# Kernel optimization log

Measured on AMD Instinct MI355X. Metric: run time of the kernel, lower is better.

The kernel has to match this reference:

```python
import jax, jax.numpy as jnp
import numpy as np

H, D = 8, 32
IN, HID, OUT = 256, 256, 128
N_PAR, N_FIG, N_TAB, N_CIT = 100000, 20000, 20000, 50000
E = 200000


def setup_inputs() -> dict:
    key = jax.random.key(0)
    ks = iter(jax.random.split(key, 80))
    def nrm(shape, s=0.05):
        return jax.random.normal(next(ks), shape, dtype=jnp.float32) * s
    def ridx(n):
        return jax.random.randint(next(ks), (E,), 0, n, dtype=jnp.int32)
    inp = {
        'x_par': nrm((N_PAR, IN), 1.0), 'x_fig': nrm((N_FIG, IN), 1.0),
        'x_tab': nrm((N_TAB, IN), 1.0), 'x_cit': nrm((N_CIT, IN), 1.0),
    }
    for t in ['par', 'fig', 'tab', 'cit']:
        inp[f'Wp_{t}'] = nrm((IN, HID)); inp[f'bp_{t}'] = nrm((HID,))
    for et in ['pf', 'fp', 'pt', 'tp', 'pc', 'cp']:
        inp[f'a_{et}_s'] = nrm((H, D)); inp[f'a_{et}_d'] = nrm((H, D))
    inp['k_w'] = nrm((HID, HID)); inp['k_b'] = nrm((HID,)); inp['q'] = nrm((HID,))
    for t in ['par', 'fig', 'tab', 'cit']:
        inp[f'Wh_{t}'] = nrm((HID, OUT)); inp[f'bh_{t}'] = nrm((OUT,))
    inp['cls_w'] = nrm((2 * OUT, 1)); inp['cls_b'] = nrm((1,))
    inp['pf_src'] = ridx(N_PAR); inp['pf_dst'] = ridx(N_FIG)
    inp['fp_src'] = ridx(N_FIG); inp['fp_dst'] = ridx(N_PAR)
    inp['pt_src'] = ridx(N_PAR); inp['pt_dst'] = ridx(N_TAB)
    inp['tp_src'] = ridx(N_TAB); inp['tp_dst'] = ridx(N_PAR)
    inp['pc_src'] = ridx(N_PAR); inp['pc_dst'] = ridx(N_CIT)
    inp['cp_src'] = ridx(N_CIT); inp['cp_dst'] = ridx(N_PAR)
    inp['target_node_idx'] = 5
    return inp


def _agg(xs, xd, si, di, a_s, a_d, n_dst):
    # HANConv metapath aggregation: GAT-style attention + per-dst softmax + scatter-sum + relu
    as_ = jnp.einsum('nhd,hd->nh', xs, a_s)            # [Ns,H]
    ad_ = jnp.einsum('nhd,hd->nh', xd, a_d)            # [Nd,H]
    alpha = jax.nn.leaky_relu(as_[si] + ad_[di], 0.2)  # [E,H]
    m = jax.ops.segment_max(alpha, di, num_segments=n_dst)
    m = jnp.where(jnp.isfinite(m), m, 0.0)
    ex = jnp.exp(alpha - m[di])
    den = jax.ops.segment_sum(ex, di, num_segments=n_dst)
    w = ex / (den[di] + 1e-16)
    out = jax.ops.segment_sum(xs[si] * w[:, :, None], di, num_segments=n_dst)  # [Nd,H,D]
    return jax.nn.relu(out.reshape(n_dst, H * D))


def _group(outs, q, kw, kb):
    # HANConv semantic (metapath-level) attention
    st = jnp.stack(outs)                               # [M,N,F]
    kmean = jnp.tanh(st @ kw + kb).mean(axis=1)        # [M,F]
    attn = jax.nn.softmax(kmean @ q)                   # [M]
    return jnp.einsum('m,mnf->nf', attn, st)


def reference(x_par, x_fig, x_tab, x_cit,
              Wp_par, bp_par, Wp_fig, bp_fig, Wp_tab, bp_tab, Wp_cit, bp_cit,
              a_pf_s, a_pf_d, a_fp_s, a_fp_d, a_pt_s, a_pt_d,
              a_tp_s, a_tp_d, a_pc_s, a_pc_d, a_cp_s, a_cp_d,
              k_w, k_b, q,
              Wh_par, bh_par, Wh_fig, bh_fig, Wh_tab, bh_tab, Wh_cit, bh_cit,
              cls_w, cls_b,
              pf_src, pf_dst, fp_src, fp_dst, pt_src, pt_dst,
              tp_src, tp_dst, pc_src, pc_dst, cp_src, cp_dst,
              target_node_idx):
    # per-node-type input projection
    h_par = (x_par @ Wp_par + bp_par).reshape(-1, H, D)
    h_fig = (x_fig @ Wp_fig + bp_fig).reshape(-1, H, D)
    h_tab = (x_tab @ Wp_tab + bp_tab).reshape(-1, H, D)
    h_cit = (x_cit @ Wp_cit + bp_cit).reshape(-1, H, D)
    # per-metapath message passing, grouped per destination node type
    o_fig = _group([_agg(h_par, h_fig, pf_src, pf_dst, a_pf_s, a_pf_d, N_FIG)], q, k_w, k_b)
    o_tab = _group([_agg(h_par, h_tab, pt_src, pt_dst, a_pt_s, a_pt_d, N_TAB)], q, k_w, k_b)
    o_cit = _group([_agg(h_par, h_cit, pc_src, pc_dst, a_pc_s, a_pc_d, N_CIT)], q, k_w, k_b)
    o_par = _group([
        _agg(h_fig, h_par, fp_src, fp_dst, a_fp_s, a_fp_d, N_PAR),
        _agg(h_tab, h_par, tp_src, tp_dst, a_tp_s, a_tp_d, N_PAR),
        _agg(h_cit, h_par, cp_src, cp_dst, a_cp_s, a_cp_d, N_PAR),
    ], q, k_w, k_b)
    # output heads (table/cited_paper heads computed in the original but unused for scores)
    par_emb = o_par @ Wh_par + bh_par
    fig_emb = o_fig @ Wh_fig + bh_fig
    _ = o_tab @ Wh_tab + bh_tab
    _ = o_cit @ Wh_cit + bh_cit
    # pairwise classifier: target figure embedding broadcast against every paragraph
    target = fig_emb[target_node_idx]
    comb = jnp.concatenate(
        [jnp.broadcast_to(target[None, :], (par_emb.shape[0], OUT)), par_emb], axis=1)
    scores = (comb @ cls_w + cls_b)[:, 0]
    return scores
```

## Files before the change

kernel.cpp:

```cpp
#include <hip/hip_runtime.h>
#include <hip/hip_bf16.h>
#include <math.h>

typedef float f32x4 __attribute__((ext_vector_type(4)));
typedef short bf16x8 __attribute__((ext_vector_type(8)));

#define NPAR 100000
#define NFIG 20000
#define NTAB 20000
#define NCIT 50000
#define NEDGE 200000
#define CAP 32
#define PFCAP 79

__device__ __forceinline__ unsigned short f2b(float f) {
    union { float f; unsigned u; } x; x.f = f;
    unsigned r = x.u + 0x7FFFu + ((x.u >> 16) & 1u);
    return (unsigned short)(r >> 16);
}
__device__ __forceinline__ float b2f(unsigned short b) {
    union { unsigned u; float f; } x; x.u = ((unsigned)b) << 16; return x.f;
}
__device__ __forceinline__ float fast_tanh(float x) {
    float e = __expf(2.f * x);
    return 1.f - 2.f * __builtin_amdgcn_rcpf(e + 1.f);
}
__device__ __forceinline__ void async_copy16(const unsigned short* g, unsigned short* l) {
    __builtin_amdgcn_global_load_lds(
        (const __attribute__((address_space(1))) unsigned int*)g,
        (__attribute__((address_space(3))) unsigned int*)l, 16, 0, 0);
}

__global__ void k_transpose5(const float* __restrict__ W0, const float* __restrict__ W1,
                             const float* __restrict__ W2, const float* __restrict__ W3,
                             const float* __restrict__ W4, unsigned short* __restrict__ WT) {
    int b = blockIdx.x, which = b >> 8, k = b & 255, n = threadIdx.x;
    const float* W = which == 0 ? W0 : which == 1 ? W1 : which == 2 ? W2 : which == 3 ? W3 : W4;
    WT[(size_t)which * 65536 + n * 256 + k] = f2b(W[k * 256 + n]);
}

__global__ void k_precompute(const float* __restrict__ WhF, const float* __restrict__ bhF,
                             const float* __restrict__ WhP, const float* __restrict__ bhP,
                             const float* __restrict__ clsw, const float* __restrict__ clsb,
                             float* __restrict__ u, float* __restrict__ v, float* __restrict__ smallb) {
    int t = threadIdx.x;
    float su = 0.f, sv = 0.f;
    for (int j = 0; j < 128; ++j) {
        su += WhF[t * 128 + j] * clsw[j];
        sv += WhP[t * 128 + j] * clsw[128 + j];
    }
    u[t] = su; v[t] = sv;
    if (t == 0) {
        float c = clsb[0];
        for (int j = 0; j < 128; ++j) c += bhF[j] * clsw[j] + bhP[j] * clsw[128 + j];
        smallb[264] = c;
    }
}

__global__ void k_edges(const int* __restrict__ d0, const int* __restrict__ d1,
                        const int* __restrict__ d2, int* __restrict__ count,
                        int* __restrict__ elist,
                        const int* __restrict__ psrc, const int* __restrict__ pdst,
                        const int* __restrict__ tgtp, int* __restrict__ mlist) {
    int b = blockIdx.x;
    int m = b / 782;
    int e = (b - m * 782) * 256 + threadIdx.x;
    if (e >= NEDGE) return;
    if (m < 3) {
        const int* dst = m == 0 ? d0 : m == 1 ? d1 : d2;
        int d = dst[e];
        int* cnt = count + (size_t)m * NPAR;
        int* el = elist + (size_t)m * NPAR * CAP;
        int slot = atomicAdd(&cnt[d], 1);
        if (slot < CAP) el[(size_t)d * CAP + slot] = e;
    } else {
        if (pdst[e] == tgtp[0]) {
            int slot = atomicAdd(&mlist[0], 1);
            if (slot < PFCAP) mlist[1 + slot] = psrc[e];
        }
    }
}

struct ProjPack {
    const float* X[4];
    const unsigned short* WT[4];
    const float* bias[4];
    unsigned short* H[4];
    const float* av[16];
    float* ov[16];
    int nrows[4];
    int bbase[4];
    int nv[4];
};

#define LOADA(k0, A0, A1) do { \
    const float4* _p = reinterpret_cast<const float4*>(Arow + (k0)); \
    A0 = _p[0]; A1 = _p[1]; } while (0)
#define WRITEA(buf, A0, A1) do { \
    __align__(16) unsigned short _t[8]; \
    _t[0] = f2b(A0.x); _t[1] = f2b(A0.y); _t[2] = f2b(A0.z); _t[3] = f2b(A0.w); \
    _t[4] = f2b(A1.x); _t[5] = f2b(A1.y); _t[6] = f2b(A1.z); _t[7] = f2b(A1.w); \
    *reinterpret_cast<uint4*>(&As[buf][arow * 32 + acol]) = *reinterpret_cast<const uint4*>(_t); } while (0)

__global__ __launch_bounds__(512, 4) void k_gemm_proj(ProjPack p) {
    __shared__ __align__(16) unsigned short As[2][128 * 32];
    __shared__ __align__(16) unsigned short Bs[2][256 * 32];
    int bid = blockIdx.x;
    int ty = (bid >= p.bbase[1]) + (bid >= p.bbase[2]) + (bid >= p.bbase[3]);
    int m0 = (bid - p.bbase[ty]) * 128;
    const float* Xf = p.X[ty];
    const unsigned short* B = p.WT[ty];
    unsigned short* Hout = p.H[ty];
    int Nrows = p.nrows[ty];
    int nv = p.nv[ty];

    int t = threadIdx.x, l = t & 63, w = t >> 6;
    int wm = (w >> 2) * 64, wn = (w & 3) * 64;
    int lr = l & 15, hi = l >> 4;
    int arow = t >> 2, acol = (t & 3) * 8;
    int arow_c = m0 + arow; if (arow_c > Nrows - 1) arow_c = Nrows - 1;
    const float* Arow = Xf + (size_t)arow_c * 256 + acol;
    f32x4 acc[4][4] = {};
    float4 aP0, aP1, aQ0, aQ1;

    auto stageB = [&](int buf, int k0) {
#pragma unroll
        for (int i = 0; i < 2; ++i) {
            int rowb = w * 32 + i * 16;
            async_copy16(B + (size_t)(rowb + (l >> 2)) * 256 + k0 + (l & 3) * 8,
                         &Bs[buf][rowb * 32]);
        }
    };

    LOADA(0, aP0, aP1);
    stageB(0, 0);
    WRITEA(0, aP0, aP1);
    LOADA(32, aQ0, aQ1);
    asm volatile("s_waitcnt vmcnt(2) lgkmcnt(0)" ::: "memory");
    __builtin_amdgcn_s_barrier();

#pragma unroll
    for (int ks = 0; ks < 8; ++ks) {
        int cur = ks & 1;
        if (ks < 7) stageB(cur ^ 1, (ks + 1) * 32);
        if (ks < 6) {
            if ((ks & 1) == 0) LOADA((ks + 2) * 32, aP0, aP1);
            else               LOADA((ks + 2) * 32, aQ0, aQ1);
        }
        bf16x8 af[4], bfr[4];
#pragma unroll
        for (int mm = 0; mm < 4; ++mm)
            af[mm] = *reinterpret_cast<const bf16x8*>(&As[cur][(wm + mm * 16 + lr) * 32 + hi * 8]);
#pragma unroll
        for (int nn = 0; nn < 4; ++nn)
            bfr[nn] = *reinterpret_cast<const bf16x8*>(&Bs[cur][(wn + nn * 16 + lr) * 32 + hi * 8]);
#pragma unroll
        for (int mm = 0; mm < 4; ++mm)
#pragma unroll
            for (int nn = 0; nn < 4; ++nn)
                acc[mm][nn] = __builtin_amdgcn_mfma_f32_16x16x32_bf16(bfr[nn], af[mm], acc[mm][nn], 0, 0, 0);
        if (ks < 7) {
            if ((ks & 1) == 0) WRITEA(cur ^ 1, aQ0, aQ1);
            else               WRITEA(cur ^ 1, aP0, aP1);
            if (ks < 6) asm volatile("s_waitcnt vmcnt(2) lgkmcnt(0)" ::: "memory");
            else        asm volatile("s_waitcnt vmcnt(0) lgkmcnt(0)" ::: "memory");
            __builtin_amdgcn_s_barrier();
        }
    }

    __syncthreads();
    float* sattp = (float*)&As[0][0];
    unsigned short* Hst = &Bs[0][0];

    float4 bv4[4], av4[4][4];
#pragma unroll
    for (int nn = 0; nn < 4; ++nn)
        bv4[nn] = *reinterpret_cast<const float4*>(p.bias[ty] + wn + nn * 16 + hi * 4);
#pragma unroll
    for (int v = 0; v < 4; ++v)
        if (v < nv) {
            const float* A = p.av[ty * 4 + v];
#pragma unroll
            for (int nn = 0; nn < 4; ++nn)
                av4[v][nn] = *reinterpret_cast<const float4*>(A + wn + nn * 16 + hi * 4);
        }
    int h0 = (w & 3) * 2;
#pragma unroll
    for (int mm = 0; mm < 4; ++mm) {
        int lrow = wm + mm * 16 + lr;
        float sv[4][2] = {};
#pragma unroll
        for (int nn = 0; nn < 4; ++nn) {
            float c0 = acc[mm][nn][0] + bv4[nn].x;
            float c1 = acc[mm][nn][1] + bv4[nn].y;
            float c2 = acc[mm][nn][2] + bv4[nn].z;
            float c3 = acc[mm][nn][3] + bv4[nn].w;
#pragma unroll
            for (int v = 0; v < 4; ++v)
                if (v < nv)
                    sv[v][nn >> 1] += c0 * av4[v][nn].x + c1 * av4[v][nn].y +
                                      c2 * av4[v][nn].z + c3 * av4[v][nn].w;
        }
#pragma unroll
        for (int v = 0; v < 4; ++v)
            if (v < nv) {
#pragma unroll
                for (int hp = 0; hp < 2; ++hp) {
                    float s = sv[v][hp];
                    s += __shfl_xor(s, 16); s += __shfl_xor(s, 32);
                    if (hi == 0) sattp[v * 1024 + lrow * 8 + h0 + hp] = s;
                }
            }
    }

    if (ty != 0) {
        for (int hf = 0; hf < 2; ++hf) {
            if ((w >> 2) == hf) {
#pragma unroll
                for (int mm = 0; mm < 4; ++mm) {
                    int lr2 = mm * 16 + lr;
                    int swz = (lr2 & 7) << 4;
#pragma unroll
                    for (int nn = 0; nn < 4; ++nn) {
                        int colb = (wn + nn * 16 + hi * 4) * 2;
                        ushort4 o;
                        o.x = f2b(acc[mm][nn][0] + bv4[nn].x);
                        o.y = f2b(acc[mm][nn][1] + bv4[nn].y);
                        o.z = f2b(acc[mm][nn][2] + bv4[nn].z);
                        o.w = f2b(acc[mm][nn][3] + bv4[nn].w);
                        *reinterpret_cast<ushort4*>((char*)Hst + lr2 * 512 + (colb ^ swz)) = o;
                    }
                }
            }
            __syncthreads();
            {
                int row = t >> 3;
                int g = m0 + hf * 64 + row;
                if (g < Nrows) {
                    int swz = (row & 7) << 4;
#pragma unroll
                    for (int pass = 0; pass < 4; ++pass) {
                        int c = (t & 7) + pass * 8;
                        uint4 val = *reinterpret_cast<const uint4*>(
                            (const char*)Hst + row * 512 + ((c * 16) ^ swz));
                        *reinterpret_cast<uint4*>(Hout + (size_t)g * 256 + c * 8) = val;
                    }
                }
            }
            __syncthreads();
        }
    } else {
        __syncthreads();
    }

    for (int i = t; i < nv * 1024; i += 512) {
        int v = i >> 10, rem = i & 1023, lrow = rem >> 3, hd = rem & 7;
        int g = m0 + lrow;
        if (g < Nrows) p.ov[ty * 4 + v][(size_t)g * 8 + hd] = sattp[v * 1024 + lrow * 8 + hd];
    }
}

__global__ void k_pf_proj(const int* __restrict__ mlist, const float* __restrict__ Xp,
                          const unsigned short* __restrict__ WTp, const float* __restrict__ bp,
                          unsigned short* __restrict__ Hs) {
    int b = blockIdx.x;
    int cnt = mlist[0]; if (cnt > PFCAP) cnt = PFCAP;
    if (b >= cnt) return;
    int s = mlist[1 + b];
    __shared__ float xr[256];
    int t = threadIdx.x;
    xr[t] = Xp[(size_t)s * 256 + t];
    __syncthreads();
    const unsigned short* wrow = WTp + (size_t)t * 256;
    float acc = bp[t];
    for (int k = 0; k < 256; k += 8) {
        uint4 wv = *reinterpret_cast<const uint4*>(wrow + k);
        unsigned wsv[4] = { wv.x, wv.y, wv.z, wv.w };
#pragma unroll
        for (int j = 0; j < 4; ++j) {
            acc += xr[k + j * 2]     * b2f((unsigned short)(wsv[j] & 0xffffu));
            acc += xr[k + j * 2 + 1] * b2f((unsigned short)(wsv[j] >> 16));
        }
    }
    Hs[(size_t)b * 256 + t] = f2b(acc);
}

struct GKPack {
    const int* src[3]; const int* count[3]; const int* elist[3];
    const unsigned short* H[3]; const float* as_[3]; const float* ad_[3];
    const unsigned short* Bw; const float* kb; const float* v;
    float* ksum[3]; float* gout[3];
};
__global__ __launch_bounds__(512, 4) void k_gather_kmean(GKPack p) {
    __shared__ __align__(16) unsigned short Ar[32 * 256];
    __shared__ __align__(16) unsigned short Bs[2][256 * 32];
    int bid = blockIdx.x;
    int m = bid / 3125, b2 = bid - m * 3125;
    const int* src = p.src[m];
    const int* count = p.count[m];
    const int* elist = p.elist[m];
    const unsigned short* Hsrc = p.H[m];
    const float* as_ = p.as_[m];
    const float* ad_ = p.ad_[m];
    const unsigned short* Bw = p.Bw;
    int t = threadIdx.x, l = t & 63, w = t >> 6;
    int m0 = b2 * 32;
    int lg = l & 15, gb = l & 48;
    float* ks_rep = p.ksum[m] + (size_t)(b2 & 7) * 256;

    auto stageB = [&](int buf, int k0) {
#pragma unroll
        for (int i = 0; i < 2; ++i) {
            int rowb = w * 32 + i * 16;
            async_copy16(Bw + (size_t)(rowb + (l >> 2)) * 256 + k0 + (((l & 3) ^ ((l >> 2) & 3)) * 8),
                         &Bs[buf][rowb * 32]);
        }
    };
    stageB(0, 0);

    int ld = w * 4 + (l >> 4);
    int d = m0 + ld;
    int cnt = count[d]; if (cnt > CAP) cnt = CAP;
    int e1 = (lg < cnt) ? elist[(size_t)d * CAP + lg] : -1;
    int e2 = (lg + 16 < cnt) ? elist[(size_t)d * CAP + lg + 16] : -1;
    int s1 = (e1 >= 0) ? src[e1] : 0;
    int s2 = (e2 >= 0) ? src[e2] : 0;
    float adh = ad_[d * 8 + (lg >> 1)];

    float4 vv0 = *reinterpret_cast<const float4*>(p.v + lg * 16);
    float4 vv1 = *reinterpret_cast<const float4*>(p.v + lg * 16 + 4);
    float4 vv2 = *reinterpret_cast<const float4*>(p.v + lg * 16 + 8);
    float4 vv3 = *reinterpret_cast<const float4*>(p.v + lg * 16 + 12);
    float vr[16] = { vv0.x, vv0.y, vv0.z, vv0.w, vv1.x, vv1.y, vv1.z, vv1.w,
                     vv2.x, vv2.y, vv2.z, vv2.w, vv3.x, vv3.y, vv3.z, vv3.w };

    {
        float ar[16];
#pragma unroll
        for (int k = 0; k < 16; ++k) ar[k] = 0.f;
        float den = 0.f;
        int sC = __shfl(s1, gb);
        const uint4* hp0 = reinterpret_cast<const uint4*>(Hsrc + (size_t)sC * 256 + lg * 16);
        uint4 hA = {}, hB = {};
        float asv = 0.f;
        if (cnt > 0) { hA = hp0[0]; hB = hp0[1]; asv = as_[sC * 8 + (lg >> 1)]; }
        for (int i = 0; i < cnt; ++i) {
            int iN = i + 1;
            uint4 nA = {}, nB = {};
            float nas = 0.f;
            if (iN < cnt) {
                int sN = (iN < 16) ? __shfl(s1, gb + (iN & 15)) : __shfl(s2, gb + ((iN - 16) & 15));
                const uint4* np = reinterpret_cast<const uint4*>(Hsrc + (size_t)sN * 256 + lg * 16);
                nA = np[0]; nB = np[1];
                nas = as_[sN * 8 + (lg >> 1)];
            }
            float al = asv + adh;
            al = al > 0.f ? al : 0.2f * al;
            float ex = __expf(al); den += ex;
            unsigned wds[8] = { hA.x, hA.y, hA.z, hA.w, hB.x, hB.y, hB.z, hB.w };
#pragma unroll
            for (int k = 0; k < 8; ++k) {
                ar[k * 2]     += ex * b2f((unsigned short)(wds[k] & 0xffffu));
                ar[k * 2 + 1] += ex * b2f((unsigned short)(wds[k] >> 16));
            }
            hA = nA; hB = nB; asv = nas;
        }
        float inv = 1.f / (den + 1e-16f);
        float gs = 0.f;
        __align__(16) unsigned short ob[16];
#pragma unroll
        for (int k = 0; k < 16; ++k) {
            float r = fmaxf(ar[k] * inv, 0.f);
            gs += r * vr[k];
            ob[k] = f2b(r);
        }
        int u0 = (lg * 2) ^ (ld & 7), u1 = (lg * 2 + 1) ^ (ld & 7);
        *reinterpret_cast<uint4*>(&Ar[ld * 256 + u0 * 8]) = *reinterpret_cast<const uint4*>(ob);
        *reinterpret_cast<uint4*>(&Ar[ld * 256 + u1 * 8]) = *reinterpret_cast<const uint4*>(ob + 8);
        gs += __shfl_xor(gs, 1); gs += __shfl_xor(gs, 2); gs += __shfl_xor(gs, 4); gs += __shfl_xor(gs, 8);
        if (lg == 0) p.gout[m][d] = gs;
    }
    __syncthreads();

    int wm = (w >> 2) * 16, wn = (w & 3) * 64, lr = l & 15, hi = l >> 4;
    f32x4 acc[4] = {};
#pragma unroll
    for (int ks = 0; ks < 8; ++ks) {
        int cur = ks & 1;
        if (ks < 7) stageB(cur ^ 1, (ks + 1) * 32);
        bf16x8 af, bfr[4];
        {
            int rr = wm + lr;
            af = *reinterpret_cast<const bf16x8*>(&Ar[rr * 256 + (((ks * 4 + hi) ^ (rr & 7)) * 8)]);
        }
#pragma unroll
        for (int nn = 0; nn < 4; ++nn) {
            int row = wn + nn * 16 + lr;
            bfr[nn] = *reinterpret_cast<const bf16x8*>(&Bs[cur][row * 32 + ((hi ^ (row & 3)) * 8)]);
        }
#pragma unroll
        for (int nn = 0; nn < 4; ++nn)
            acc[nn] = __builtin_amdgcn_mfma_f32_16x16x32_bf16(af, bfr[nn], acc[nn], 0, 0, 0);
        if (ks < 7) {
            asm volatile("s_waitcnt vmcnt(0)" ::: "memory");
            __builtin_amdgcn_s_barrier();
        }
    }
#pragma unroll
    for (int nn = 0; nn < 4; ++nn) {
        int col = wn + nn * 16 + lr;
        float kbv = p.kb[col];
        float cs = 0.f;
#pragma unroll
        for (int r = 0; r < 4; ++r)
            cs += fast_tanh(acc[nn][r] + kbv);
        cs += __shfl_xor(cs, 16);
        cs += __shfl_xor(cs, 32);
        if (hi == 0) atomicAdd(&ks_rep[col], cs);
    }
}

__global__ void k_pf_acc(const int* __restrict__ mlist, const int* __restrict__ tgtp,
                         const unsigned short* __restrict__ Hs,
                         const float* __restrict__ as_pf, const float* __restrict__ ad_pf,
                         float* __restrict__ smallb) {
    __shared__ float sacc[4][256];
    __shared__ float sden[4][8];
    int t = threadIdx.x, w = t >> 6, l = t & 63;
    int tgt = tgtp[0];
    int cnt = mlist[0]; if (cnt > PFCAP) cnt = PFCAP;
    int h = l >> 3;
    float adh = ad_pf[tgt * 8 + h];
    float a0 = 0.f, a1 = 0.f, a2 = 0.f, a3 = 0.f, den = 0.f;
    for (int i = w; i < cnt; i += 4) {
        int s = mlist[1 + i];
        float al = as_pf[s * 8 + h] + adh;
        al = al > 0.f ? al : 0.2f * al;
        float ex = __expf(al);
        ushort4 hv = *reinterpret_cast<const ushort4*>(&Hs[(size_t)i * 256 + l * 4]);
        a0 += ex * b2f(hv.x); a1 += ex * b2f(hv.y); a2 += ex * b2f(hv.z); a3 += ex * b2f(hv.w);
        den += ex;
    }
    sacc[w][l * 4 + 0] = a0; sacc[w][l * 4 + 1] = a1;
    sacc[w][l * 4 + 2] = a2; sacc[w][l * 4 + 3] = a3;
    if ((l & 7) == 0) sden[w][h] = den;
    __syncthreads();
    smallb[t] = sacc[0][t] + sacc[1][t] + sacc[2][t] + sacc[3][t];
    if (t < 8) smallb[256 + t] = sden[0][t] + sden[1][t] + sden[2][t] + sden[3][t];
}

__global__ void k_finalize(const float* __restrict__ kacc, const float* __restrict__ q,
                           const float* __restrict__ u, float* __restrict__ smallb) {
    __shared__ float red[256];
    __shared__ float sm[3];
    int t = threadIdx.x;
    float qv = q[t];
    for (int m = 0; m < 3; ++m) {
        float acc = 0.f;
#pragma unroll
        for (int rep = 0; rep < 8; ++rep) acc += kacc[m * 2048 + rep * 256 + t];
        red[t] = acc * qv;
        __syncthreads();
        for (int s = 128; s > 0; s >>= 1) { if (t < s) red[t] += red[t + s]; __syncthreads(); }
        if (t == 0) sm[m] = red[0] / (float)NPAR;
        __syncthreads();
    }
    float den = smallb[256 + (t >> 5)];
    float rt = fmaxf(smallb[t] / (den + 1e-16f), 0.f);
    red[t] = rt * u[t];
    __syncthreads();
    for (int s = 128; s > 0; s >>= 1) { if (t < s) red[t] += red[t + s]; __syncthreads(); }
    if (t == 0) {
        float mx = fmaxf(sm[0], fmaxf(sm[1], sm[2]));
        float e0 = expf(sm[0] - mx), e1 = expf(sm[1] - mx), e2 = expf(sm[2] - mx);
        float sd = e0 + e1 + e2;
        smallb[265] = e0 / sd; smallb[266] = e1 / sd; smallb[267] = e2 / sd;
        smallb[268] = red[0] + smallb[264];
    }
}

__global__ void k_scores(const float* __restrict__ g, const float* __restrict__ smallb,
                         float* __restrict__ out) {
    int i = blockIdx.x * 256 + threadIdx.x;
    if (i >= NPAR) return;
    out[i] = smallb[268] + smallb[265] * g[i] + smallb[266] * g[NPAR + i] + smallb[267] * g[2 * NPAR + i];
}

extern "C" void kernel_launch(void* const* d_in, const int* in_sizes, int n_in,
                              void* d_out, int out_size, void* d_ws, size_t ws_size,
                              hipStream_t stream) {
    char* base = (char*)d_ws;
    size_t off = 0;
    auto alloc = [&](size_t b) -> void* { void* p = base + off; off += (b + 255) & ~(size_t)255; return p; };

    unsigned short* Hsmall = (unsigned short*)alloc((size_t)PFCAP * 256 * 2);
    unsigned short* h_fig = (unsigned short*)alloc((size_t)NFIG * 256 * 2);
    unsigned short* h_tab = (unsigned short*)alloc((size_t)NTAB * 256 * 2);
    unsigned short* h_cit = (unsigned short*)alloc((size_t)NCIT * 256 * 2);
    unsigned short* WTall = (unsigned short*)alloc((size_t)5 * 65536 * 2);
    unsigned short* WT_par = WTall, *WT_fig = WTall + 65536, *WT_tab = WTall + 2 * 65536,
                  *WT_cit = WTall + 3 * 65536, *kwT = WTall + 4 * 65536;
    float* as_pf = (float*)alloc((size_t)NPAR * 8 * 4);
    float* ad_fp = (float*)alloc((size_t)NPAR * 8 * 4);
    float* ad_tp = (float*)alloc((size_t)NPAR * 8 * 4);
    float* ad_cp = (float*)alloc((size_t)NPAR * 8 * 4);
    float* as_fp = (float*)alloc((size_t)NFIG * 8 * 4);
    float* ad_pf = (float*)alloc((size_t)NFIG * 8 * 4);
    float* as_tp = (float*)alloc((size_t)NTAB * 8 * 4);
    float* as_cp = (float*)alloc((size_t)NCIT * 8 * 4);
    float* gbuf  = (float*)alloc((size_t)3 * NPAR * 4);
    int* count3  = (int*)alloc((size_t)3 * NPAR * 4);
    int* elist3  = (int*)alloc((size_t)3 * NPAR * CAP * 4);
    float* kacc  = (float*)alloc((size_t)3 * 8 * 256 * 4);
    float* smallb = (float*)alloc(512 * 4);
    int* mlist   = (int*)alloc((1 + PFCAP) * 4);
    float* uvec  = (float*)alloc(256 * 4);
    float* vvec  = (float*)alloc(256 * 4);

    hipMemsetAsync(kacc, 0, 24576 + 2048 + 512, stream);
    hipMemsetAsync(count3, 0, (size_t)3 * NPAR * 4, stream);

    k_transpose5<<<5 * 256, 256, 0, stream>>>((const float*)d_in[4], (const float*)d_in[6],
                                              (const float*)d_in[8], (const float*)d_in[10],
                                              (const float*)d_in[24], WTall);

    k_precompute<<<1, 256, 0, stream>>>((const float*)d_in[29], (const float*)d_in[30],
                                        (const float*)d_in[27], (const float*)d_in[28],
                                        (const float*)d_in[35], (const float*)d_in[36],
                                        uvec, vvec, smallb);

    k_edges<<<4 * 782, 256, 0, stream>>>((const int*)d_in[40], (const int*)d_in[44],
                                         (const int*)d_in[48], count3, elist3,
                                         (const int*)d_in[37], (const int*)d_in[38],
                                         (const int*)d_in[49], mlist);
    k_pf_proj<<<PFCAP, 256, 0, stream>>>(mlist, (const float*)d_in[0], WT_par,
                                         (const float*)d_in[5], Hsmall);

    ProjPack pp;
    pp.X[0] = (const float*)d_in[0]; pp.X[1] = (const float*)d_in[1];
    pp.X[2] = (const float*)d_in[2]; pp.X[3] = (const float*)d_in[3];
    pp.WT[0] = WT_par; pp.WT[1] = WT_fig; pp.WT[2] = WT_tab; pp.WT[3] = WT_cit;
    pp.bias[0] = (const float*)d_in[5]; pp.bias[1] = (const float*)d_in[7];
    pp.bias[2] = (const float*)d_in[9]; pp.bias[3] = (const float*)d_in[11];
    pp.H[0] = h_fig; pp.H[1] = h_fig; pp.H[2] = h_tab; pp.H[3] = h_cit;
    pp.nrows[0] = NPAR; pp.nrows[1] = NFIG; pp.nrows[2] = NTAB; pp.nrows[3] = NCIT;
    pp.bbase[0] = 0; pp.bbase[1] = 782; pp.bbase[2] = 939; pp.bbase[3] = 1096;
    pp.nv[0] = 4; pp.nv[1] = 2; pp.nv[2] = 1; pp.nv[3] = 1;
    for (int i = 0; i < 16; ++i) { pp.av[i] = nullptr; pp.ov[i] = nullptr; }
    pp.av[0] = (const float*)d_in[12]; pp.ov[0] = as_pf;
    pp.av[1] = (const float*)d_in[15]; pp.ov[1] = ad_fp;
    pp.av[2] = (const float*)d_in[19]; pp.ov[2] = ad_tp;
    pp.av[3] = (const float*)d_in[23]; pp.ov[3] = ad_cp;
    pp.av[4] = (const float*)d_in[14]; pp.ov[4] = as_fp;
    pp.av[5] = (const float*)d_in[13]; pp.ov[5] = ad_pf;
    pp.av[8] = (const float*)d_in[18]; pp.ov[8] = as_tp;
    pp.av[12] = (const float*)d_in[22]; pp.ov[12] = as_cp;
    k_gemm_proj<<<1487, 512, 0, stream>>>(pp);

    k_pf_acc<<<1, 256, 0, stream>>>(mlist, (const int*)d_in[49], Hsmall, as_pf, ad_pf, smallb);

    GKPack gk;
    gk.src[0] = (const int*)d_in[39]; gk.src[1] = (const int*)d_in[43]; gk.src[2] = (const int*)d_in[47];
    gk.count[0] = count3; gk.count[1] = count3 + NPAR; gk.count[2] = count3 + 2 * NPAR;
    gk.elist[0] = elist3; gk.elist[1] = elist3 + (size_t)NPAR * CAP; gk.elist[2] = elist3 + (size_t)2 * NPAR * CAP;
    gk.H[0] = h_fig; gk.H[1] = h_tab; gk.H[2] = h_cit;
    gk.as_[0] = as_fp; gk.as_[1] = as_tp; gk.as_[2] = as_cp;
    gk.ad_[0] = ad_fp; gk.ad_[1] = ad_tp; gk.ad_[2] = ad_cp;
    gk.Bw = kwT; gk.kb = (const float*)d_in[25]; gk.v = vvec;
    gk.ksum[0] = kacc; gk.ksum[1] = kacc + 2048; gk.ksum[2] = kacc + 4096;
    gk.gout[0] = gbuf; gk.gout[1] = gbuf + NPAR; gk.gout[2] = gbuf + 2 * NPAR;
    k_gather_kmean<<<3 * 3125, 512, 0, stream>>>(gk);

    k_finalize<<<1, 256, 0, stream>>>(kacc, (const float*)d_in[26], uvec, smallb);
    k_scores<<<391, 256, 0, stream>>>(gbuf, smallb, (float*)d_out);
}
```

Baseline: 360.9 us.

## Process all three metapaths per block in gather-kmean kernel to reuse staged weights

Merges the three per-metapath block groups into one block that gathers and aggregates each of the three metapaths for the same 32 destination nodes, storing three A tiles in shared memory. The k_w tile is then staged once and fed to three MFMA accumulator sets, cutting redundant weight loads and block launches. The cost is triple the A-tile shared memory and more registers, which can lower occupancy and serialize the latency-bound gather loops within each block.

```diff
diff --git a/kernel.cpp b/kernel.cpp
--- a/kernel.cpp
+++ b/kernel.cpp
@@ -292,21 +292,13 @@
     float* ksum[3]; float* gout[3];
 };
 __global__ __launch_bounds__(512, 4) void k_gather_kmean(GKPack p) {
-    __shared__ __align__(16) unsigned short Ar[32 * 256];
+    __shared__ __align__(16) unsigned short Ar[3][32 * 256];
     __shared__ __align__(16) unsigned short Bs[2][256 * 32];
-    int bid = blockIdx.x;
-    int m = bid / 3125, b2 = bid - m * 3125;
-    const int* src = p.src[m];
-    const int* count = p.count[m];
-    const int* elist = p.elist[m];
-    const unsigned short* Hsrc = p.H[m];
-    const float* as_ = p.as_[m];
-    const float* ad_ = p.ad_[m];
+    int b2 = blockIdx.x;
     const unsigned short* Bw = p.Bw;
     int t = threadIdx.x, l = t & 63, w = t >> 6;
     int m0 = b2 * 32;
     int lg = l & 15, gb = l & 48;
-    float* ks_rep = p.ksum[m] + (size_t)(b2 & 7) * 256;
 
     auto stageB = [&](int buf, int k0) {
 #pragma unroll
@@ -320,12 +312,6 @@
 
     int ld = w * 4 + (l >> 4);
     int d = m0 + ld;
-    int cnt = count[d]; if (cnt > CAP) cnt = CAP;
-    int e1 = (lg < cnt) ? elist[(size_t)d * CAP + lg] : -1;
-    int e2 = (lg + 16 < cnt) ? elist[(size_t)d * CAP + lg + 16] : -1;
-    int s1 = (e1 >= 0) ? src[e1] : 0;
-    int s2 = (e2 >= 0) ? src[e2] : 0;
-    float adh = ad_[d * 8 + (lg >> 1)];
 
     float4 vv0 = *reinterpret_cast<const float4*>(p.v + lg * 16);
     float4 vv1 = *reinterpret_cast<const float4*>(p.v + lg * 16 + 4);
@@ -334,7 +320,17 @@
     float vr[16] = { vv0.x, vv0.y, vv0.z, vv0.w, vv1.x, vv1.y, vv1.z, vv1.w,
                      vv2.x, vv2.y, vv2.z, vv2.w, vv3.x, vv3.y, vv3.z, vv3.w };
 
-    {
+    for (int mp = 0; mp < 3; ++mp) {
+        const int* src = p.src[mp];
+        const unsigned short* Hsrc = p.H[mp];
+        const float* as_ = p.as_[mp];
+        int cnt = p.count[mp][d]; if (cnt > CAP) cnt = CAP;
+        int e1 = (lg < cnt) ? p.elist[mp][(size_t)d * CAP + lg] : -1;
+        int e2 = (lg + 16 < cnt) ? p.elist[mp][(size_t)d * CAP + lg + 16] : -1;
+        int s1 = (e1 >= 0) ? src[e1] : 0;
+        int s2 = (e2 >= 0) ? src[e2] : 0;
+        float adh = p.ad_[mp][d * 8 + (lg >> 1)];
+
         float ar[16];
 #pragma unroll
         for (int k = 0; k < 16; ++k) ar[k] = 0.f;
@@ -375,32 +371,36 @@
             ob[k] = f2b(r);
         }
         int u0 = (lg * 2) ^ (ld & 7), u1 = (lg * 2 + 1) ^ (ld & 7);
-        *reinterpret_cast<uint4*>(&Ar[ld * 256 + u0 * 8]) = *reinterpret_cast<const uint4*>(ob);
-        *reinterpret_cast<uint4*>(&Ar[ld * 256 + u1 * 8]) = *reinterpret_cast<const uint4*>(ob + 8);
+        *reinterpret_cast<uint4*>(&Ar[mp][ld * 256 + u0 * 8]) = *reinterpret_cast<const uint4*>(ob);
+        *reinterpret_cast<uint4*>(&Ar[mp][ld * 256 + u1 * 8]) = *reinterpret_cast<const uint4*>(ob + 8);
         gs += __shfl_xor(gs, 1); gs += __shfl_xor(gs, 2); gs += __shfl_xor(gs, 4); gs += __shfl_xor(gs, 8);
-        if (lg == 0) p.gout[m][d] = gs;
+        if (lg == 0) p.gout[mp][d] = gs;
     }
     __syncthreads();
 
     int wm = (w >> 2) * 16, wn = (w & 3) * 64, lr = l & 15, hi = l >> 4;
-    f32x4 acc[4] = {};
+    f32x4 acc0[4] = {}, acc1[4] = {}, acc2[4] = {};
 #pragma unroll
     for (int ks = 0; ks < 8; ++ks) {
         int cur = ks & 1;
         if (ks < 7) stageB(cur ^ 1, (ks + 1) * 32);
-        bf16x8 af, bfr[4];
-        {
-            int rr = wm + lr;
-            af = *reinterpret_cast<const bf16x8*>(&Ar[rr * 256 + (((ks * 4 + hi) ^ (rr & 7)) * 8)]);
-        }
+        int rr = wm + lr;
+        int aoff = rr * 256 + (((ks * 4 + hi) ^ (rr & 7)) * 8);
+        bf16x8 a0 = *reinterpret_cast<const bf16x8*>(&Ar[0][aoff]);
+        bf16x8 a1 = *reinterpret_cast<const bf16x8*>(&Ar[1][aoff]);
+        bf16x8 a2 = *reinterpret_cast<const bf16x8*>(&Ar[2][aoff]);
+        bf16x8 bfr[4];
 #pragma unroll
         for (int nn = 0; nn < 4; ++nn) {
             int row = wn + nn * 16 + lr;
             bfr[nn] = *reinterpret_cast<const bf16x8*>(&Bs[cur][row * 32 + ((hi ^ (row & 3)) * 8)]);
         }
 #pragma unroll
-        for (int nn = 0; nn < 4; ++nn)
-            acc[nn] = __builtin_amdgcn_mfma_f32_16x16x32_bf16(af, bfr[nn], acc[nn], 0, 0, 0);
+        for (int nn = 0; nn < 4; ++nn) {
+            acc0[nn] = __builtin_amdgcn_mfma_f32_16x16x32_bf16(a0, bfr[nn], acc0[nn], 0, 0, 0);
+            acc1[nn] = __builtin_amdgcn_mfma_f32_16x16x32_bf16(a1, bfr[nn], acc1[nn], 0, 0, 0);
+            acc2[nn] = __builtin_amdgcn_mfma_f32_16x16x32_bf16(a2, bfr[nn], acc2[nn], 0, 0, 0);
+        }
         if (ks < 7) {
             asm volatile("s_waitcnt vmcnt(0)" ::: "memory");
             __builtin_amdgcn_s_barrier();
@@ -410,13 +410,22 @@
     for (int nn = 0; nn < 4; ++nn) {
         int col = wn + nn * 16 + lr;
         float kbv = p.kb[col];
-        float cs = 0.f;
-#pragma unroll
-        for (int r = 0; r < 4; ++r)
-            cs += fast_tanh(acc[nn][r] + kbv);
-        cs += __shfl_xor(cs, 16);
-        cs += __shfl_xor(cs, 32);
-        if (hi == 0) atomicAdd(&ks_rep[col], cs);
+        float cs0 = 0.f, cs1 = 0.f, cs2 = 0.f;
+#pragma unroll
+        for (int r = 0; r < 4; ++r) {
+            cs0 += fast_tanh(acc0[nn][r] + kbv);
+            cs1 += fast_tanh(acc1[nn][r] + kbv);
+            cs2 += fast_tanh(acc2[nn][r] + kbv);
+        }
+        cs0 += __shfl_xor(cs0, 16); cs0 += __shfl_xor(cs0, 32);
+        cs1 += __shfl_xor(cs1, 16); cs1 += __shfl_xor(cs1, 32);
+        cs2 += __shfl_xor(cs2, 16); cs2 += __shfl_xor(cs2, 32);
+        if (hi == 0) {
+            int rep = (b2 & 7) * 256 + col;
+            atomicAdd(&p.ksum[0][rep], cs0);
+            atomicAdd(&p.ksum[1][rep], cs1);
+            atomicAdd(&p.ksum[2][rep], cs2);
+        }
     }
 }
 
@@ -569,7 +578,7 @@
     gk.Bw = kwT; gk.kb = (const float*)d_in[25]; gk.v = vvec;
     gk.ksum[0] = kacc; gk.ksum[1] = kacc + 2048; gk.ksum[2] = kacc + 4096;
     gk.gout[0] = gbuf; gk.gout[1] = gbuf + NPAR; gk.gout[2] = gbuf + 2 * NPAR;
-    k_gather_kmean<<<3 * 3125, 512, 0, stream>>>(gk);
+    k_gather_kmean<<<3125, 512, 0, stream>>>(gk);
 
     k_finalize<<<1, 256, 0, stream>>>(kacc, (const float*)d_in[26], uvec, smallb);
     k_scores<<<391, 256, 0, stream>>>(gbuf, smallb, (float*)d_out);
```

Result: faster. 339.5 us (-5.9%).
